# Performance work log

Measured on AMD Instinct MI355X. Metric: run time of the kernel, lower is better.

The kernel has to match this reference:

```python
import jax, jax.numpy as jnp
import numpy as np

N_NODES = 170000
N_EDGES = 1200000
IN_DIM = 64
OUT_DIM = 40


def setup_inputs() -> dict:
    key = jax.random.key(0)
    k1, k2, k3, k4 = jax.random.split(key, 4)
    feats = jax.random.normal(k1, (N_NODES, IN_DIM), dtype=jnp.float32)
    # Linear layer params (Kaiming-ish scale)
    W = jax.random.normal(k2, (OUT_DIM, IN_DIM), dtype=jnp.float32) * (1.0 / np.sqrt(IN_DIM))
    b = jnp.zeros((OUT_DIM,), dtype=jnp.float32)
    src = jax.random.randint(k3, (N_EDGES,), 0, N_NODES, dtype=jnp.int64)
    dst = jax.random.randint(k4, (N_EDGES,), 0, N_NODES, dtype=jnp.int64)
    return {"feats": feats, "W": W, "b": b, "src": src, "dst": dst}


def reference(feats, W, b, src, dst):
    # DGL SGConv, k=1: symmetric normalization by in-degree^-1/2 on both sides.
    n = feats.shape[0]
    deg = jax.ops.segment_sum(jnp.ones_like(dst, dtype=feats.dtype), dst, num_segments=n)
    norm = jax.lax.rsqrt(jnp.maximum(deg, 1.0))  # clamp(min=1)
    h = feats * norm[:, None]                    # [N, D] pre-scale
    msgs = jnp.take(h, src, axis=0)              # [E, D] gather
    agg = jax.ops.segment_sum(msgs, dst, num_segments=n)  # [N, D] scatter-sum
    h = agg * norm[:, None]                      # post-scale
    out = jnp.einsum('nd,cd->nc', h, W) + b      # Linear(IN_DIM -> OUT_DIM)
    return out
```

## Files before the change

kernel.cpp:

```cpp
#include <hip/hip_runtime.h>
#include <hip/hip_bf16.h>

#define N_NODES 170000
#define N_EDGES 1200000
#define IN_DIM 64
#define OUT_DIM 40
#define PAD 32
#define ZW 20
#define MTILES (N_NODES / 16)
#define TFB ((MTILES + 3) / 4)
#define SEGS 8
#define SEG_SZ (N_NODES / SEGS)
#define SLICES 512
#define SLICE_E ((N_EDGES + SLICES - 1) / SLICES)
#define FILLB (SLICES * SEGS)
#define FUSED_BLOCKS (FILLB + TFB)
#define GWAVES (N_NODES / 2)
#define PRER 5
#define WS_DS32_OFF 36056576ULL
#define WS_SS32_OFF (WS_DS32_OFF + (size_t)N_EDGES * 4)
#define WS_NEED     (WS_SS32_OFF + (size_t)N_EDGES * 4)

typedef __attribute__((ext_vector_type(8))) short short8;
typedef __attribute__((ext_vector_type(4))) float f32x4;

__device__ __forceinline__ float bf2f(unsigned int u) {
    union { unsigned int i; float f; } v;
    v.i = u << 16;
    return v.f;
}

__device__ __forceinline__ unsigned short f2bf_bits(float x) {
    __hip_bfloat16 h = __float2bfloat16(x);
    union { __hip_bfloat16 h; unsigned short u; } c; c.h = h;
    return c.u;
}

__device__ __forceinline__ int load_idx(const void* p, int e, int is_i32) {
    return is_i32 ? ((const int*)p)[e] : (int)((const long long*)p)[e];
}

__global__ void __launch_bounds__(256) k_init(
    const unsigned short* __restrict__ Wraw, const unsigned short* __restrict__ braw,
    const unsigned int* __restrict__ dstraw, const unsigned int* __restrict__ srcraw,
    int* __restrict__ flags, unsigned short* __restrict__ Wb, float* __restrict__ bfv,
    int* __restrict__ cnt, int* __restrict__ ds32, int* __restrict__ ss32) {
    int tid = blockIdx.x * 256 + threadIdx.x;
    int gsz = (int)gridDim.x * 256;
    int4* c4 = (int4*)cnt;
    for (int i = tid; i < 42500; i += gsz) c4[i] = make_int4(0, 0, 0, 0);

    __shared__ int s_i32l;
    if (threadIdx.x == 0) s_i32l = 0;
    __syncthreads();
    if (dstraw[2 * threadIdx.x + 1] != 0u) atomicOr(&s_i32l, 1);
    __syncthreads();
    int is_i32 = s_i32l;

    if (!is_i32 && ds32) {
        const long long* d64 = (const long long*)dstraw;
        const long long* s64 = (const long long*)srcraw;
        for (int i = tid; i < N_EDGES; i += gsz) ds32[i] = (int)d64[i];
        for (int i = tid; i < N_EDGES; i += gsz) ss32[i] = (int)s64[i];
    }
    if (blockIdx.x != 0) return;

    __shared__ int s_f32;
    if (threadIdx.x == 0) s_f32 = 0;
    __syncthreads();
    for (int i = threadIdx.x; i < OUT_DIM * IN_DIM; i += 256) {
        float v = bf2f(Wraw[i]);
        if (!(fabsf(v) <= 100.0f)) atomicOr(&s_f32, 1);
    }
    __syncthreads();
    int is_f32 = s_f32;
    if (threadIdx.x == 0) { flags[0] = s_f32; flags[1] = is_i32; }
    for (int i = threadIdx.x; i < OUT_DIM * IN_DIM; i += 256)
        Wb[i] = is_f32 ? f2bf_bits(((const float*)Wraw)[i]) : Wraw[i];
    for (int i = threadIdx.x; i < OUT_DIM; i += 256)
        bfv[i] = is_f32 ? ((const float*)braw)[i] : bf2f(braw[i]);
}

__global__ void __launch_bounds__(256) k_fused(
    const void* __restrict__ src, const void* __restrict__ dst,
    int* __restrict__ cnt, int* __restrict__ slots,
    const void* __restrict__ feats, const unsigned short* __restrict__ Wb,
    unsigned short* __restrict__ Zp16, const int* __restrict__ flags,
    const int* __restrict__ ds32, const int* __restrict__ ss32) {
    int bid = blockIdx.x;
    int do_fill, id;
    if (bid < 2 * TFB) { do_fill = bid & 1; id = bid >> 1; }
    else               { do_fill = 1;       id = bid - TFB; }

    if (do_fill) {
        int is_i32 = flags[1];
        int seg   = id & 7;
        int slice = id >> 3;
        int lo = seg * SEG_SZ, hi = lo + SEG_SZ;
        int e0 = slice * SLICE_E;
        int e1 = e0 + SLICE_E; if (e1 > N_EDGES) e1 = N_EDGES;
        const int* dp = is_i32 ? (const int*)dst : ds32;
        const int* sp = is_i32 ? (const int*)src : ss32;
        if (dp) {
            int nE = e1 - e0;
            int nV = nE >> 2;
            const int4* dv = (const int4*)(dp + e0);
            const int4* sv = (const int4*)(sp + e0);
            for (int q = (int)threadIdx.x; q < nV; q += 256) {
                int4 d4 = dv[q];
                int4 s4 = sv[q];
                if (d4.x >= lo && d4.x < hi) {
                    int pos = atomicAdd(&cnt[d4.x], 1);
                    if (pos < PAD) slots[(size_t)d4.x * PAD + pos] = s4.x;
                }
                if (d4.y >= lo && d4.y < hi) {
                    int pos = atomicAdd(&cnt[d4.y], 1);
                    if (pos < PAD) slots[(size_t)d4.y * PAD + pos] = s4.y;
                }
                if (d4.z >= lo && d4.z < hi) {
                    int pos = atomicAdd(&cnt[d4.z], 1);
                    if (pos < PAD) slots[(size_t)d4.z * PAD + pos] = s4.z;
                }
                if (d4.w >= lo && d4.w < hi) {
                    int pos = atomicAdd(&cnt[d4.w], 1);
                    if (pos < PAD) slots[(size_t)d4.w * PAD + pos] = s4.w;
                }
            }
            int rem = nE & 3;
            if ((int)threadIdx.x < rem) {
                int e = e0 + (nV << 2) + (int)threadIdx.x;
                int d = dp[e];
                if (d >= lo && d < hi) {
                    int pos = atomicAdd(&cnt[d], 1);
                    if (pos < PAD) slots[(size_t)d * PAD + pos] = sp[e];
                }
            }
        } else {
            for (int e = e0 + (int)threadIdx.x; e < e1; e += 256) {
                int d = load_idx(dst, e, 0);
                if (d >= lo && d < hi) {
                    int s = load_idx(src, e, 0);
                    int pos = atomicAdd(&cnt[d], 1);
                    if (pos < PAD) slots[(size_t)d * PAD + pos] = s;
                }
            }
        }
    } else {
        int is_f32 = flags[0];
        int wave = id * 4 + (int)(threadIdx.x >> 6);
        int lane = threadIdx.x & 63;
        if (wave >= MTILES) return;
        int m = lane & 15;
        int quad = lane >> 4;
        int node0 = wave * 16;

        short8 a0, a1;
        if (is_f32) {
            const float* frow = (const float*)feats + (size_t)(node0 + m) * IN_DIM + quad * 8;
            float4 p0 = *(const float4*)(frow + 0);
            float4 p1 = *(const float4*)(frow + 4);
            float4 p2 = *(const float4*)(frow + 32);
            float4 p3 = *(const float4*)(frow + 36);
            a0[0] = (short)f2bf_bits(p0.x); a0[1] = (short)f2bf_bits(p0.y);
            a0[2] = (short)f2bf_bits(p0.z); a0[3] = (short)f2bf_bits(p0.w);
            a0[4] = (short)f2bf_bits(p1.x); a0[5] = (short)f2bf_bits(p1.y);
            a0[6] = (short)f2bf_bits(p1.z); a0[7] = (short)f2bf_bits(p1.w);
            a1[0] = (short)f2bf_bits(p2.x); a1[1] = (short)f2bf_bits(p2.y);
            a1[2] = (short)f2bf_bits(p2.z); a1[3] = (short)f2bf_bits(p2.w);
            a1[4] = (short)f2bf_bits(p3.x); a1[5] = (short)f2bf_bits(p3.y);
            a1[6] = (short)f2bf_bits(p3.z); a1[7] = (short)f2bf_bits(p3.w);
        } else {
            const unsigned short* frow = (const unsigned short*)feats + (size_t)(node0 + m) * IN_DIM + quad * 8;
            a0 = *(const short8*)(frow);
            a1 = *(const short8*)(frow + 32);
        }

        f32x4 c0 = {0.f, 0.f, 0.f, 0.f}, c1 = c0, c2 = c0;
#pragma unroll
        for (int t = 0; t < 3; t++) {
            int n = t * 16 + m;
            bool ok = (n < OUT_DIM);
            short8 b0, b1;
#pragma unroll
            for (int j = 0; j < 8; j++) { b0[j] = 0; b1[j] = 0; }
            if (ok) {
                const unsigned short* wrow = Wb + (size_t)n * IN_DIM + quad * 8;
                b0 = *(const short8*)(wrow);
                b1 = *(const short8*)(wrow + 32);
            }
            if (t == 0) {
                c0 = __builtin_amdgcn_mfma_f32_16x16x32_bf16(a0, b0, c0, 0, 0, 0);
                c0 = __builtin_amdgcn_mfma_f32_16x16x32_bf16(a1, b1, c0, 0, 0, 0);
            } else if (t == 1) {
                c1 = __builtin_amdgcn_mfma_f32_16x16x32_bf16(a0, b0, c1, 0, 0, 0);
                c1 = __builtin_amdgcn_mfma_f32_16x16x32_bf16(a1, b1, c1, 0, 0, 0);
            } else {
                c2 = __builtin_amdgcn_mfma_f32_16x16x32_bf16(a0, b0, c2, 0, 0, 0);
                c2 = __builtin_amdgcn_mfma_f32_16x16x32_bf16(a1, b1, c2, 0, 0, 0);
            }
        }

        int r0 = quad * 4;
#pragma unroll
        for (int r = 0; r < 4; r++) {
            size_t base = (size_t)(node0 + r0 + r) * OUT_DIM;
            Zp16[base + m]      = f2bf_bits(c0[r]);
            Zp16[base + 16 + m] = f2bf_bits(c1[r]);
            if (m < 8)
                Zp16[base + 32 + m] = f2bf_bits(c2[r]);
        }
    }
}

__global__ void __launch_bounds__(256) k_gather(
    const int* __restrict__ cnt, const int* __restrict__ slots,
    const unsigned int* __restrict__ Zp, const float* __restrict__ bfv,
    float* __restrict__ out) {
    int wid = (blockIdx.x * blockDim.x + threadIdx.x) >> 6;
    int lane = threadIdx.x & 63;
    if (wid >= GWAVES) return;
    int nA = wid * 2, nB = nA + 1;

    int deg_my = cnt[nA + (lane >> 5)];
    int deg_ot = __shfl(deg_my, lane ^ 32);
    int degA = (lane < 32) ? deg_my : deg_ot;
    int degB = (lane < 32) ? deg_ot : deg_my;
    int dcA = degA > PAD ? PAD : degA;
    int dcB = degB > PAD ? PAD : degB;
    int dcm = dcA > dcB ? dcA : dcB;

    int myslot = slots[(size_t)(nA + (lane >> 5)) * PAD + (lane & 31)];

    int grp = lane / 10;
    int g3 = grp - (grp >= 3 ? 3 : 0);
    int cidx = lane - grp * 10;
    bool lact = (grp < 6);
    int side = (grp >= 3);
    int dcS = side ? dcB : dcA;
    int sbase = side * 32;

    float a0 = 0.f, a1 = 0.f, a2 = 0.f, a3 = 0.f;

    uint2 rr[PRER];
    int   cd[PRER];
    int   vv[PRER];
#pragma unroll
    for (int rd = 0; rd < PRER; rd++) {
        vv[rd] = 0;
        if (rd * 3 < dcm) {
            int e1 = rd * 3 + g3;
            bool v1 = lact && (e1 < dcS);
            int s1 = __shfl(myslot, sbase + (v1 ? e1 : 0));
            s1 = v1 ? s1 : 0;
            rr[rd] = *(const uint2*)(Zp + (size_t)s1 * ZW + 2 * cidx);
            cd[rd] = cnt[s1];
            vv[rd] = v1 ? 1 : 0;
        }
    }
#pragma unroll
    for (int rd = 0; rd < PRER; rd++) {
        if (rd * 3 < dcm && vv[rd]) {
            float nvs = rsqrtf(cd[rd] > 1 ? (float)cd[rd] : 1.0f);
            a0 = fmaf(bf2f(rr[rd].x & 0xFFFFu), nvs, a0);
            a1 = fmaf(bf2f(rr[rd].x >> 16),     nvs, a1);
            a2 = fmaf(bf2f(rr[rd].y & 0xFFFFu), nvs, a2);
            a3 = fmaf(bf2f(rr[rd].y >> 16),     nvs, a3);
        }
    }
    for (int rd = PRER; rd * 3 < dcm; rd++) {
        int e1 = rd * 3 + g3;
        bool v1 = lact && (e1 < dcS);
        int s1 = __shfl(myslot, sbase + (v1 ? e1 : 0));
        s1 = v1 ? s1 : 0;
        uint2 r = *(const uint2*)(Zp + (size_t)s1 * ZW + 2 * cidx);
        int cn = cnt[s1];
        if (v1) {
            float nvs = rsqrtf(cn > 1 ? (float)cn : 1.0f);
            a0 = fmaf(bf2f(r.x & 0xFFFFu), nvs, a0);
            a1 = fmaf(bf2f(r.x >> 16),     nvs, a1);
            a2 = fmaf(bf2f(r.y & 0xFFFFu), nvs, a2);
            a3 = fmaf(bf2f(r.y >> 16),     nvs, a3);
        }
    }

    float t0 = a0 + __shfl(a0, (lane + 10) & 63) + __shfl(a0, (lane + 20) & 63);
    float t1 = a1 + __shfl(a1, (lane + 10) & 63) + __shfl(a1, (lane + 20) & 63);
    float t2 = a2 + __shfl(a2, (lane + 10) & 63) + __shfl(a2, (lane + 20) & 63);
    float t3 = a3 + __shfl(a3, (lane + 10) & 63) + __shfl(a3, (lane + 20) & 63);

    bool wA = (lane < 10);
    bool wB = (lane >= 30 && lane < 40);
    if (wA || wB) {
        int nOut = wA ? nA : nB;
        int ci   = wA ? lane : (lane - 30);
        int dg   = wA ? degA : degB;
        float nv = rsqrtf(dg > 1 ? (float)dg : 1.0f);
        float4 o;
        o.x = fmaf(t0, nv, bfv[4 * ci + 0]);
        o.y = fmaf(t1, nv, bfv[4 * ci + 1]);
        o.z = fmaf(t2, nv, bfv[4 * ci + 2]);
        o.w = fmaf(t3, nv, bfv[4 * ci + 3]);
        *reinterpret_cast<float4*>(out + (size_t)nOut * OUT_DIM + 4 * ci) = o;
    }
}

extern "C" void kernel_launch(void* const* d_in, const int* in_sizes, int n_in,
                              void* d_out, int out_size, void* d_ws, size_t ws_size,
                              hipStream_t stream) {
    const void* feats = d_in[0];
    const void* W     = d_in[1];
    const void* b     = d_in[2];
    const void* src   = d_in[3];
    const void* dst   = d_in[4];

    char* ws = (char*)d_ws;
    int*            flags = (int*)(ws + 0);
    float*          bfv   = (float*)(ws + 256);
    unsigned short* Wb    = (unsigned short*)(ws + 1024);
    int*            cnt   = (int*)(ws + 16384);
    int*            slots = (int*)(ws + 696448);
    unsigned short* Zp16  = (unsigned short*)(ws + 22456448);
    unsigned int*   Zp    = (unsigned int*)(ws + 22456448);
    int*            ds32  = (ws_size >= WS_NEED) ? (int*)(ws + WS_DS32_OFF) : nullptr;
    int*            ss32  = (ws_size >= WS_NEED) ? (int*)(ws + WS_SS32_OFF) : nullptr;

    k_init<<<1024, 256, 0, stream>>>((const unsigned short*)W, (const unsigned short*)b,
                                     (const unsigned int*)dst, (const unsigned int*)src,
                                     flags, Wb, bfv, cnt, ds32, ss32);
    k_fused<<<FUSED_BLOCKS, 256, 0, stream>>>(src, dst, cnt, slots, feats, Wb, Zp16, flags, ds32, ss32);
    k_gather<<<(GWAVES * 64 + 255) / 256, 256, 0, stream>>>(cnt, slots, Zp, bfv, (float*)d_out);
}
```

Baseline: 191.0 us.

## Drop init kernel, detect dtypes inline, widen gather loads to 8 channels

```diff
diff --git a/kernel.cpp b/kernel.cpp
--- a/kernel.cpp
+++ b/kernel.cpp
@@ -16,10 +16,7 @@
 #define FILLB (SLICES * SEGS)
 #define FUSED_BLOCKS (FILLB + TFB)
 #define GWAVES (N_NODES / 2)
-#define PRER 5
-#define WS_DS32_OFF 36056576ULL
-#define WS_SS32_OFF (WS_DS32_OFF + (size_t)N_EDGES * 4)
-#define WS_NEED     (WS_SS32_OFF + (size_t)N_EDGES * 4)
+#define PRER 3
 
 typedef __attribute__((ext_vector_type(8))) short short8;
 typedef __attribute__((ext_vector_type(4))) float f32x4;
@@ -36,72 +33,34 @@
     return c.u;
 }
 
-__device__ __forceinline__ int load_idx(const void* p, int e, int is_i32) {
-    return is_i32 ? ((const int*)p)[e] : (int)((const long long*)p)[e];
-}
-
-__global__ void __launch_bounds__(256) k_init(
-    const unsigned short* __restrict__ Wraw, const unsigned short* __restrict__ braw,
-    const unsigned int* __restrict__ dstraw, const unsigned int* __restrict__ srcraw,
-    int* __restrict__ flags, unsigned short* __restrict__ Wb, float* __restrict__ bfv,
-    int* __restrict__ cnt, int* __restrict__ ds32, int* __restrict__ ss32) {
-    int tid = blockIdx.x * 256 + threadIdx.x;
-    int gsz = (int)gridDim.x * 256;
-    int4* c4 = (int4*)cnt;
-    for (int i = tid; i < 42500; i += gsz) c4[i] = make_int4(0, 0, 0, 0);
-
-    __shared__ int s_i32l;
-    if (threadIdx.x == 0) s_i32l = 0;
-    __syncthreads();
-    if (dstraw[2 * threadIdx.x + 1] != 0u) atomicOr(&s_i32l, 1);
-    __syncthreads();
-    int is_i32 = s_i32l;
-
-    if (!is_i32 && ds32) {
-        const long long* d64 = (const long long*)dstraw;
-        const long long* s64 = (const long long*)srcraw;
-        for (int i = tid; i < N_EDGES; i += gsz) ds32[i] = (int)d64[i];
-        for (int i = tid; i < N_EDGES; i += gsz) ss32[i] = (int)s64[i];
-    }
-    if (blockIdx.x != 0) return;
-
-    __shared__ int s_f32;
-    if (threadIdx.x == 0) s_f32 = 0;
-    __syncthreads();
-    for (int i = threadIdx.x; i < OUT_DIM * IN_DIM; i += 256) {
-        float v = bf2f(Wraw[i]);
-        if (!(fabsf(v) <= 100.0f)) atomicOr(&s_f32, 1);
-    }
-    __syncthreads();
-    int is_f32 = s_f32;
-    if (threadIdx.x == 0) { flags[0] = s_f32; flags[1] = is_i32; }
-    for (int i = threadIdx.x; i < OUT_DIM * IN_DIM; i += 256)
-        Wb[i] = is_f32 ? f2bf_bits(((const float*)Wraw)[i]) : Wraw[i];
-    for (int i = threadIdx.x; i < OUT_DIM; i += 256)
-        bfv[i] = is_f32 ? ((const float*)braw)[i] : bf2f(braw[i]);
-}
-
 __global__ void __launch_bounds__(256) k_fused(
     const void* __restrict__ src, const void* __restrict__ dst,
     int* __restrict__ cnt, int* __restrict__ slots,
-    const void* __restrict__ feats, const unsigned short* __restrict__ Wb,
-    unsigned short* __restrict__ Zp16, const int* __restrict__ flags,
-    const int* __restrict__ ds32, const int* __restrict__ ss32) {
+    const void* __restrict__ feats, const unsigned short* __restrict__ Wraw,
+    const unsigned short* __restrict__ braw, float* __restrict__ bfv,
+    unsigned short* __restrict__ Zp16) {
     int bid = blockIdx.x;
     int do_fill, id;
     if (bid < 2 * TFB) { do_fill = bid & 1; id = bid >> 1; }
     else               { do_fill = 1;       id = bid - TFB; }
 
+    __shared__ int sh_flag;
+    if (threadIdx.x == 0) sh_flag = 0;
+    __syncthreads();
+
     if (do_fill) {
-        int is_i32 = flags[1];
+        if (((const unsigned int*)dst)[2 * threadIdx.x + 1] != 0u) atomicOr(&sh_flag, 1);
+        __syncthreads();
+        int is_i32 = sh_flag;
+
         int seg   = id & 7;
         int slice = id >> 3;
         int lo = seg * SEG_SZ, hi = lo + SEG_SZ;
         int e0 = slice * SLICE_E;
         int e1 = e0 + SLICE_E; if (e1 > N_EDGES) e1 = N_EDGES;
-        const int* dp = is_i32 ? (const int*)dst : ds32;
-        const int* sp = is_i32 ? (const int*)src : ss32;
-        if (dp) {
+        if (is_i32) {
+            const int* dp = (const int*)dst;
+            const int* sp = (const int*)src;
             int nE = e1 - e0;
             int nV = nE >> 2;
             const int4* dv = (const int4*)(dp + e0);
@@ -136,17 +95,28 @@
                 }
             }
         } else {
+            const long long* dp = (const long long*)dst;
+            const long long* sp = (const long long*)src;
             for (int e = e0 + (int)threadIdx.x; e < e1; e += 256) {
-                int d = load_idx(dst, e, 0);
+                int d = (int)dp[e];
                 if (d >= lo && d < hi) {
-                    int s = load_idx(src, e, 0);
+                    int s = (int)sp[e];
                     int pos = atomicAdd(&cnt[d], 1);
                     if (pos < PAD) slots[(size_t)d * PAD + pos] = s;
                 }
             }
         }
     } else {
-        int is_f32 = flags[0];
+        for (int i = threadIdx.x; i < OUT_DIM * IN_DIM; i += 256) {
+            float v = bf2f(Wraw[i]);
+            if (!(fabsf(v) <= 100.0f)) atomicOr(&sh_flag, 1);
+        }
+        __syncthreads();
+        int is_f32 = sh_flag;
+        if (bid == 0 && threadIdx.x < OUT_DIM)
+            bfv[threadIdx.x] = is_f32 ? ((const float*)braw)[threadIdx.x]
+                                      : bf2f(braw[threadIdx.x]);
+
         int wave = id * 4 + (int)(threadIdx.x >> 6);
         int lane = threadIdx.x & 63;
         if (wave >= MTILES) return;
@@ -184,9 +154,25 @@
 #pragma unroll
             for (int j = 0; j < 8; j++) { b0[j] = 0; b1[j] = 0; }
             if (ok) {
-                const unsigned short* wrow = Wb + (size_t)n * IN_DIM + quad * 8;
-                b0 = *(const short8*)(wrow);
-                b1 = *(const short8*)(wrow + 32);
+                if (is_f32) {
+                    const float* wrow = (const float*)Wraw + (size_t)n * IN_DIM + quad * 8;
+                    float4 w0 = *(const float4*)(wrow + 0);
+                    float4 w1 = *(const float4*)(wrow + 4);
+                    float4 w2 = *(const float4*)(wrow + 32);
+                    float4 w3 = *(const float4*)(wrow + 36);
+                    b0[0] = (short)f2bf_bits(w0.x); b0[1] = (short)f2bf_bits(w0.y);
+                    b0[2] = (short)f2bf_bits(w0.z); b0[3] = (short)f2bf_bits(w0.w);
+                    b0[4] = (short)f2bf_bits(w1.x); b0[5] = (short)f2bf_bits(w1.y);
+                    b0[6] = (short)f2bf_bits(w1.z); b0[7] = (short)f2bf_bits(w1.w);
+                    b1[0] = (short)f2bf_bits(w2.x); b1[1] = (short)f2bf_bits(w2.y);
+                    b1[2] = (short)f2bf_bits(w2.z); b1[3] = (short)f2bf_bits(w2.w);
+                    b1[4] = (short)f2bf_bits(w3.x); b1[5] = (short)f2bf_bits(w3.y);
+                    b1[6] = (short)f2bf_bits(w3.z); b1[7] = (short)f2bf_bits(w3.w);
+                } else {
+                    const unsigned short* wrow = Wraw + (size_t)n * IN_DIM + quad * 8;
+                    b0 = *(const short8*)(wrow);
+                    b1 = *(const short8*)(wrow + 32);
+                }
             }
             if (t == 0) {
                 c0 = __builtin_amdgcn_mfma_f32_16x16x32_bf16(a0, b0, c0, 0, 0, 0);
@@ -231,48 +217,53 @@
 
     int myslot = slots[(size_t)(nA + (lane >> 5)) * PAD + (lane & 31)];
 
-    int grp = lane / 10;
-    int g3 = grp - (grp >= 3 ? 3 : 0);
-    int cidx = lane - grp * 10;
-    bool lact = (grp < 6);
-    int side = (grp >= 3);
+    int grp = lane / 5;
+    int cidx = lane - grp * 5;
+    bool lact = (grp < 12);
+    int side = (grp >= 6) ? 1 : 0;
+    int g6 = grp - side * 6;
     int dcS = side ? dcB : dcA;
     int sbase = side * 32;
 
     float a0 = 0.f, a1 = 0.f, a2 = 0.f, a3 = 0.f;
-
-    uint2 rr[PRER];
+    float a4 = 0.f, a5 = 0.f, a6 = 0.f, a7 = 0.f;
+
+    uint4 rr[PRER];
     int   cd[PRER];
     int   vv[PRER];
 #pragma unroll
     for (int rd = 0; rd < PRER; rd++) {
         vv[rd] = 0;
-        if (rd * 3 < dcm) {
-            int e1 = rd * 3 + g3;
+        if (rd * 6 < dcm) {
+            int e1 = rd * 6 + g6;
             bool v1 = lact && (e1 < dcS);
             int s1 = __shfl(myslot, sbase + (v1 ? e1 : 0));
             s1 = v1 ? s1 : 0;
-            rr[rd] = *(const uint2*)(Zp + (size_t)s1 * ZW + 2 * cidx);
+            rr[rd] = *(const uint4*)(Zp + (size_t)s1 * ZW + 4 * cidx);
             cd[rd] = cnt[s1];
             vv[rd] = v1 ? 1 : 0;
         }
     }
 #pragma unroll
     for (int rd = 0; rd < PRER; rd++) {
-        if (rd * 3 < dcm && vv[rd]) {
+        if (rd * 6 < dcm && vv[rd]) {
             float nvs = rsqrtf(cd[rd] > 1 ? (float)cd[rd] : 1.0f);
             a0 = fmaf(bf2f(rr[rd].x & 0xFFFFu), nvs, a0);
             a1 = fmaf(bf2f(rr[rd].x >> 16),     nvs, a1);
             a2 = fmaf(bf2f(rr[rd].y & 0xFFFFu), nvs, a2);
             a3 = fmaf(bf2f(rr[rd].y >> 16),     nvs, a3);
-        }
-    }
-    for (int rd = PRER; rd * 3 < dcm; rd++) {
-        int e1 = rd * 3 + g3;
+            a4 = fmaf(bf2f(rr[rd].z & 0xFFFFu), nvs, a4);
+            a5 = fmaf(bf2f(rr[rd].z >> 16),     nvs, a5);
+            a6 = fmaf(bf2f(rr[rd].w & 0xFFFFu), nvs, a6);
+            a7 = fmaf(bf2f(rr[rd].w >> 16),     nvs, a7);
+        }
+    }
+    for (int rd = PRER; rd * 6 < dcm; rd++) {
+        int e1 = rd * 6 + g6;
         bool v1 = lact && (e1 < dcS);
         int s1 = __shfl(myslot, sbase + (v1 ? e1 : 0));
         s1 = v1 ? s1 : 0;
-        uint2 r = *(const uint2*)(Zp + (size_t)s1 * ZW + 2 * cidx);
+        uint4 r = *(const uint4*)(Zp + (size_t)s1 * ZW + 4 * cidx);
         int cn = cnt[s1];
         if (v1) {
             float nvs = rsqrtf(cn > 1 ? (float)cn : 1.0f);
@@ -280,27 +271,37 @@
             a1 = fmaf(bf2f(r.x >> 16),     nvs, a1);
             a2 = fmaf(bf2f(r.y & 0xFFFFu), nvs, a2);
             a3 = fmaf(bf2f(r.y >> 16),     nvs, a3);
-        }
-    }
-
-    float t0 = a0 + __shfl(a0, (lane + 10) & 63) + __shfl(a0, (lane + 20) & 63);
-    float t1 = a1 + __shfl(a1, (lane + 10) & 63) + __shfl(a1, (lane + 20) & 63);
-    float t2 = a2 + __shfl(a2, (lane + 10) & 63) + __shfl(a2, (lane + 20) & 63);
-    float t3 = a3 + __shfl(a3, (lane + 10) & 63) + __shfl(a3, (lane + 20) & 63);
-
-    bool wA = (lane < 10);
-    bool wB = (lane >= 30 && lane < 40);
+            a4 = fmaf(bf2f(r.z & 0xFFFFu), nvs, a4);
+            a5 = fmaf(bf2f(r.z >> 16),     nvs, a5);
+            a6 = fmaf(bf2f(r.w & 0xFFFFu), nvs, a6);
+            a7 = fmaf(bf2f(r.w >> 16),     nvs, a7);
+        }
+    }
+
+#define RED6(A) { float s_ = A + __shfl(A, (lane + 15) & 63); \
+                  A = s_ + __shfl(s_, (lane + 5) & 63) + __shfl(s_, (lane + 10) & 63); }
+    RED6(a0) RED6(a1) RED6(a2) RED6(a3) RED6(a4) RED6(a5) RED6(a6) RED6(a7)
+#undef RED6
+
+    bool wA = (lane < 5);
+    bool wB = (lane >= 30 && lane < 35);
     if (wA || wB) {
         int nOut = wA ? nA : nB;
         int ci   = wA ? lane : (lane - 30);
         int dg   = wA ? degA : degB;
         float nv = rsqrtf(dg > 1 ? (float)dg : 1.0f);
-        float4 o;
-        o.x = fmaf(t0, nv, bfv[4 * ci + 0]);
-        o.y = fmaf(t1, nv, bfv[4 * ci + 1]);
-        o.z = fmaf(t2, nv, bfv[4 * ci + 2]);
-        o.w = fmaf(t3, nv, bfv[4 * ci + 3]);
-        *reinterpret_cast<float4*>(out + (size_t)nOut * OUT_DIM + 4 * ci) = o;
+        float* op = out + (size_t)nOut * OUT_DIM + 8 * ci;
+        float4 o1, o2;
+        o1.x = fmaf(a0, nv, bfv[8 * ci + 0]);
+        o1.y = fmaf(a1, nv, bfv[8 * ci + 1]);
+        o1.z = fmaf(a2, nv, bfv[8 * ci + 2]);
+        o1.w = fmaf(a3, nv, bfv[8 * ci + 3]);
+        o2.x = fmaf(a4, nv, bfv[8 * ci + 4]);
+        o2.y = fmaf(a5, nv, bfv[8 * ci + 5]);
+        o2.z = fmaf(a6, nv, bfv[8 * ci + 6]);
+        o2.w = fmaf(a7, nv, bfv[8 * ci + 7]);
+        *reinterpret_cast<float4*>(op)     = o1;
+        *reinterpret_cast<float4*>(op + 4) = o2;
     }
 }
 
@@ -314,19 +315,15 @@
     const void* dst   = d_in[4];
 
     char* ws = (char*)d_ws;
-    int*            flags = (int*)(ws + 0);
     float*          bfv   = (float*)(ws + 256);
-    unsigned short* Wb    = (unsigned short*)(ws + 1024);
     int*            cnt   = (int*)(ws + 16384);
     int*            slots = (int*)(ws + 696448);
     unsigned short* Zp16  = (unsigned short*)(ws + 22456448);
     unsigned int*   Zp    = (unsigned int*)(ws + 22456448);
-    int*            ds32  = (ws_size >= WS_NEED) ? (int*)(ws + WS_DS32_OFF) : nullptr;
-    int*            ss32  = (ws_size >= WS_NEED) ? (int*)(ws + WS_SS32_OFF) : nullptr;
-
-    k_init<<<1024, 256, 0, stream>>>((const unsigned short*)W, (const unsigned short*)b,
-                                     (const unsigned int*)dst, (const unsigned int*)src,
-                                     flags, Wb, bfv, cnt, ds32, ss32);
-    k_fused<<<FUSED_BLOCKS, 256, 0, stream>>>(src, dst, cnt, slots, feats, Wb, Zp16, flags, ds32, ss32);
+
+    (void)hipMemsetAsync(cnt, 0, 680000, stream);
+    k_fused<<<FUSED_BLOCKS, 256, 0, stream>>>(src, dst, cnt, slots, feats,
+                                              (const unsigned short*)W,
+                                              (const unsigned short*)b, bfv, Zp16);
     k_gather<<<(GWAVES * 64 + 255) / 256, 256, 0, stream>>>(cnt, slots, Zp, bfv, (float*)d_out);
 }
```

Measured after the change: 198.4 us. 1.04x slower.
